# Performance work log

Hardware: AMD Instinct MI355X
Metric: run time of the kernel (lower is better)

The kernel has to match this reference:

```python
import jax, jax.numpy as jnp
import numpy as np

NUM_HEAD = 16
HEAD_DIM = 64
RES_DIM = 1024
LN_EPS = 1e-5


def setup_inputs() -> dict:
    key = jax.random.key(0)
    k1, k2, k3 = jax.random.split(key, 3)
    slen, bsz = 2048, 4
    x = jax.random.normal(k1, (slen, bsz, RES_DIM), dtype=jnp.float32)
    # torch Linear weights: [out_features, in_features]
    w_qkv = jax.random.normal(k2, (NUM_HEAD * 3 * HEAD_DIM, RES_DIM), dtype=jnp.float32) * (1.0 / np.sqrt(RES_DIM))
    w_out = jax.random.normal(k3, (RES_DIM, NUM_HEAD * HEAD_DIM), dtype=jnp.float32) * (1.0 / np.sqrt(NUM_HEAD * HEAD_DIM))
    ln_w = jnp.ones((RES_DIM,), dtype=jnp.float32)
    ln_b = jnp.zeros((RES_DIM,), dtype=jnp.float32)
    return {"x": x, "w_qkv": w_qkv, "w_out": w_out, "ln_w": ln_w, "ln_b": ln_b}


def _layer_norm(x, w, b):
    mu = jnp.mean(x, axis=-1, keepdims=True)
    var = jnp.var(x, axis=-1, keepdims=True)
    return (x - mu) * jax.lax.rsqrt(var + LN_EPS) * w + b


def reference(x, w_qkv, w_out, ln_w, ln_b):
    slen, bsz, _ = x.shape
    scale = 1.0 / np.sqrt(RES_DIM).astype(np.float32)  # note: res_dim, not head_dim
    x_in = _layer_norm(x, ln_w, ln_b)  # pre_lnorm=True
    qkv = x_in @ w_qkv.T  # [s, b, n*3*d]
    qkv = qkv.reshape(slen, bsz, NUM_HEAD, 3 * HEAD_DIM)
    q, k, v = jnp.split(qkv, 3, axis=-1)  # each [s, b, n, d]
    scores = jnp.einsum('ibnd,jbnd->ijbn', q, k) * scale
    attn = jax.nn.softmax(scores, axis=1)  # softmax over keys j
    attn_out = jnp.einsum('ijbn,jbnd->ibnd', attn, v)
    attn_out = attn_out.reshape(slen, bsz, NUM_HEAD * HEAD_DIM)
    attn_out = attn_out @ w_out.T
    return x + attn_out
```

## Files before the change

kernel.cpp:

```cpp
#include <hip/hip_runtime.h>

typedef __bf16 bf16_t;
typedef __bf16 bf16x2 __attribute__((ext_vector_type(2)));
typedef __bf16 bf16x4 __attribute__((ext_vector_type(4)));
typedef __bf16 bf16x8 __attribute__((ext_vector_type(8)));
typedef float f32x4 __attribute__((ext_vector_type(4)));

#define S_LEN 2048
#define BSZ 4
#define NHEAD 16
#define HDIM 64
#define RDIM 1024
#define QKV_N 3072
#define NTOK 8192

__device__ static inline void gload_lds16(const void* g, void* l) {
    __builtin_amdgcn_global_load_lds(
        (const __attribute__((address_space(1))) void*)(unsigned long long)g,
        (__attribute__((address_space(3))) void*)(unsigned long long)l,
        16, 0, 0);
}

__global__ __launch_bounds__(256) void ln_kernel(const float* __restrict__ x,
                                                 const float* __restrict__ lw,
                                                 const float* __restrict__ lb,
                                                 bf16_t* __restrict__ xn) {
    int row = blockIdx.x;
    int tid = threadIdx.x;
    const float4* xr = (const float4*)(x + (size_t)row * RDIM);
    float4 v = xr[tid];
    float s  = v.x + v.y + v.z + v.w;
    float ss = v.x*v.x + v.y*v.y + v.z*v.z + v.w*v.w;
#pragma unroll
    for (int off = 1; off < 64; off <<= 1) {
        s  += __shfl_xor(s, off, 64);
        ss += __shfl_xor(ss, off, 64);
    }
    __shared__ float red[8];
    int wid = tid >> 6, lane = tid & 63;
    if (lane == 0) { red[wid] = s; red[wid + 4] = ss; }
    __syncthreads();
    float S  = red[0] + red[1] + red[2] + red[3];
    float SS = red[4] + red[5] + red[6] + red[7];
    float mu  = S * (1.f / RDIM);
    float var = SS * (1.f / RDIM) - mu * mu;
    float rsig = rsqrtf(var + 1e-5f);
    float4 wv = ((const float4*)lw)[tid];
    float4 bv = ((const float4*)lb)[tid];
    bf16x4 o;
    o[0] = (bf16_t)((v.x - mu) * rsig * wv.x + bv.x);
    o[1] = (bf16_t)((v.y - mu) * rsig * wv.y + bv.y);
    o[2] = (bf16_t)((v.z - mu) * rsig * wv.z + bv.z);
    o[3] = (bf16_t)((v.w - mu) * rsig * wv.w + bv.w);
    *(bf16x4*)(xn + (size_t)row * RDIM + tid * 4) = o;
}

__global__ __launch_bounds__(256) void cvt_kernel(const float* __restrict__ src,
                                                  bf16_t* __restrict__ dst, int n4) {
    int i = blockIdx.x * 256 + threadIdx.x;
    if (i < n4) {
        float4 v = ((const float4*)src)[i];
        bf16x4 o;
        o[0] = (bf16_t)v.x; o[1] = (bf16_t)v.y; o[2] = (bf16_t)v.z; o[3] = (bf16_t)v.w;
        ((bf16x4*)dst)[i] = o;
    }
}

template <int MODE>
__global__ __launch_bounds__(256) void gemm_bt_kernel(const bf16_t* __restrict__ A,
                                                      const bf16_t* __restrict__ Bm,
                                                      bf16_t* __restrict__ Cb,
                                                      const float* __restrict__ X,
                                                      float* __restrict__ Cf,
                                                      int ldc) {
    const int K = 1024;
    __shared__ bf16_t As[128 * 32];
    __shared__ bf16_t Bs[128 * 32];
    int tid = threadIdx.x;
    int lane = tid & 63, wid = tid >> 6;
    int l15 = lane & 15, lg = lane >> 4;
    int wm = wid >> 1, wn = wid & 1;
    int row0 = blockIdx.y * 128;
    int col0 = blockIdx.x * 128;

    int sr = tid >> 2;
    int sc = (tid & 3) * 8;
    const bf16_t* aSrc = A + (size_t)(row0 + sr) * K + sc;
    const bf16_t* bSrc = Bm + (size_t)(col0 + sr) * K + sc;
    bf16_t* aDst = As + tid * 8;
    bf16_t* bDst = Bs + tid * 8;

    f32x4 acc[4][4] = {};
    for (int kt = 0; kt < K; kt += 32) {
        gload_lds16(aSrc + kt, aDst);
        gload_lds16(aSrc + kt + (size_t)64 * K, aDst + 2048);
        gload_lds16(bSrc + kt, bDst);
        gload_lds16(bSrc + kt + (size_t)64 * K, bDst + 2048);
        __syncthreads();
        bf16x8 a[4], b[4];
#pragma unroll
        for (int m = 0; m < 4; m++)
            a[m] = *(const bf16x8*)(As + (wm * 64 + m * 16 + l15) * 32 + lg * 8);
#pragma unroll
        for (int n = 0; n < 4; n++)
            b[n] = *(const bf16x8*)(Bs + (wn * 64 + n * 16 + l15) * 32 + lg * 8);
#pragma unroll
        for (int m = 0; m < 4; m++)
#pragma unroll
            for (int n = 0; n < 4; n++)
                acc[m][n] = __builtin_amdgcn_mfma_f32_16x16x32_bf16(a[m], b[n], acc[m][n], 0, 0, 0);
        __syncthreads();
    }

    int crow = row0 + wm * 64 + lg * 4;
    int ccol = col0 + wn * 64 + l15;
#pragma unroll
    for (int m = 0; m < 4; m++) {
#pragma unroll
        for (int n = 0; n < 4; n++) {
#pragma unroll
            for (int r = 0; r < 4; r++) {
                int rr = crow + m * 16 + r;
                int cc = ccol + n * 16;
                size_t idx = (size_t)rr * ldc + cc;
                if (MODE == 0) {
                    Cb[idx] = (bf16_t)acc[m][n][r];
                } else {
                    Cf[idx] = acc[m][n][r] + X[idx];
                }
            }
        }
    }
}

__global__ __launch_bounds__(256) void attn_kernel(const bf16_t* __restrict__ qkv,
                                                   bf16_t* __restrict__ aout) {
    __shared__ __align__(16) bf16_t Kb[2][4096];
    __shared__ __align__(16) bf16_t VTb[2][64 * 72];
    __shared__ __align__(16) bf16_t Ps[4][16 * 88];
    int tid = threadIdx.x;
    int lane = tid & 63, wid = tid >> 6;
    int l15 = lane & 15, lg = lane >> 4;
    int b = blockIdx.y, h = blockIdx.z;
    int sq = blockIdx.x * 64 + wid * 16 + l15;

    const float scale = 0.03125f;

    const bf16_t* qbase = qkv + (size_t)(sq * 4 + b) * QKV_N + h * 192;
    bf16x8 qf0 = *(const bf16x8*)(qbase + lg * 8);
    bf16x8 qf1 = *(const bf16x8*)(qbase + 32 + lg * 8);

    int kKeyOff = lane >> 3;
    int kChunk  = (lane & 7) ^ (lane >> 3);
    int vr0 = (tid & 31) * 2;
    int vc0 = (tid >> 5) * 8;

    int sw = l15 & 7;
    int koA = ((lg ^ sw)) * 8;
    int koC = (((lg + 4) ^ sw)) * 8;

    float mrun = -3e38f, lrun = 0.f;
    f32x4 o[4] = {};

    {
        const bf16_t* ks = qkv + (size_t)(((0 + wid * 16 + kKeyOff) * 4 + b)) * QKV_N + h * 192 + 64 + kChunk * 8;
        bf16_t* kd = &Kb[0][wid * 1024 + lane * 8];
        gload_lds16(ks, kd);
        gload_lds16(ks + (size_t)8 * 4 * QKV_N, kd + 512);
        const bf16_t* vs = qkv + (size_t)((0 + vr0) * 4 + b) * QKV_N + h * 192 + 128 + vc0;
        bf16x8 v0 = *(const bf16x8*)vs;
        bf16x8 v1 = *(const bf16x8*)(vs + (size_t)4 * QKV_N);
#pragma unroll
        for (int i = 0; i < 8; i++) {
            bf16x2 pr; pr[0] = v0[i]; pr[1] = v1[i];
            *(bf16x2*)(&VTb[0][(vc0 + i) * 72 + vr0]) = pr;
        }
    }
    __syncthreads();

    int cur = 0;
    for (int t = 0; t < S_LEN / 64; t++) {
        bf16x8 v0, v1;
        bool do_stage = (t + 1) < (S_LEN / 64);
        if (do_stage) {
            int kv0 = (t + 1) * 64;
            const bf16_t* ks = qkv + (size_t)(((kv0 + wid * 16 + kKeyOff) * 4 + b)) * QKV_N + h * 192 + 64 + kChunk * 8;
            bf16_t* kd = &Kb[cur ^ 1][wid * 1024 + lane * 8];
            gload_lds16(ks, kd);
            gload_lds16(ks + (size_t)8 * 4 * QKV_N, kd + 512);
            const bf16_t* vs = qkv + (size_t)((kv0 + vr0) * 4 + b) * QKV_N + h * 192 + 128 + vc0;
            v0 = *(const bf16x8*)vs;
            v1 = *(const bf16x8*)(vs + (size_t)4 * QKV_N);
        }

        const bf16_t* kbase = &Kb[cur][l15 * 64];
        bf16x8 kfA[4], kfC[4];
#pragma unroll
        for (int kb = 0; kb < 4; kb++) {
            kfA[kb] = *(const bf16x8*)(kbase + kb * 1024 + koA);
            kfC[kb] = *(const bf16x8*)(kbase + kb * 1024 + koC);
        }
        f32x4 sc4[4];
        __builtin_amdgcn_s_setprio(1);
#pragma unroll
        for (int kb = 0; kb < 4; kb++) {
            f32x4 z = {0.f, 0.f, 0.f, 0.f};
            z = __builtin_amdgcn_mfma_f32_16x16x32_bf16(kfA[kb], qf0, z, 0, 0, 0);
            z = __builtin_amdgcn_mfma_f32_16x16x32_bf16(kfC[kb], qf1, z, 0, 0, 0);
            sc4[kb] = z;
        }
        __builtin_amdgcn_s_setprio(0);

        float tmax = sc4[0][0];
#pragma unroll
        for (int kb = 0; kb < 4; kb++)
#pragma unroll
            for (int r = 0; r < 4; r++) tmax = fmaxf(tmax, sc4[kb][r]);
        tmax = fmaxf(tmax, __shfl_xor(tmax, 16, 64));
        tmax = fmaxf(tmax, __shfl_xor(tmax, 32, 64));
        float mnew = fmaxf(mrun, tmax * scale);
        float corr = __expf(mrun - mnew);
        float lsum = 0.f;
#pragma unroll
        for (int kb = 0; kb < 4; kb++) {
            float p0 = __expf(sc4[kb][0] * scale - mnew);
            float p1 = __expf(sc4[kb][1] * scale - mnew);
            float p2 = __expf(sc4[kb][2] * scale - mnew);
            float p3 = __expf(sc4[kb][3] * scale - mnew);
            lsum += (p0 + p1) + (p2 + p3);
            bf16x4 pw;
            pw[0] = (bf16_t)p0; pw[1] = (bf16_t)p1; pw[2] = (bf16_t)p2; pw[3] = (bf16_t)p3;
            *(bf16x4*)(&Ps[wid][l15 * 88 + kb * 16 + lg * 4]) = pw;
        }
        lsum += __shfl_xor(lsum, 16, 64);
        lsum += __shfl_xor(lsum, 32, 64);
        lrun = lrun * corr + lsum;
        mrun = mnew;
#pragma unroll
        for (int dc = 0; dc < 4; dc++) {
            o[dc][0] *= corr; o[dc][1] *= corr; o[dc][2] *= corr; o[dc][3] *= corr;
        }

        if (do_stage) {
#pragma unroll
            for (int i = 0; i < 8; i++) {
                bf16x2 pr; pr[0] = v0[i]; pr[1] = v1[i];
                *(bf16x2*)(&VTb[cur ^ 1][(vc0 + i) * 72 + vr0]) = pr;
            }
        }

#pragma unroll
        for (int kc = 0; kc < 2; kc++) {
            bf16x8 pf = *(const bf16x8*)(&Ps[wid][l15 * 88 + kc * 32 + lg * 8]);
            __builtin_amdgcn_s_setprio(1);
#pragma unroll
            for (int dc = 0; dc < 4; dc++) {
                bf16x8 vf = *(const bf16x8*)(&VTb[cur][(dc * 16 + l15) * 72 + kc * 32 + lg * 8]);
                o[dc] = __builtin_amdgcn_mfma_f32_16x16x32_bf16(vf, pf, o[dc], 0, 0, 0);
            }
            __builtin_amdgcn_s_setprio(0);
        }

        __syncthreads();
        cur ^= 1;
    }

    float linv = 1.f / lrun;
    bf16_t* ob = aout + (size_t)(sq * 4 + b) * RDIM + h * 64 + lg * 4;
#pragma unroll
    for (int dc = 0; dc < 4; dc++) {
        bf16x4 ov;
        ov[0] = (bf16_t)(o[dc][0] * linv);
        ov[1] = (bf16_t)(o[dc][1] * linv);
        ov[2] = (bf16_t)(o[dc][2] * linv);
        ov[3] = (bf16_t)(o[dc][3] * linv);
        *(bf16x4*)(ob + dc * 16) = ov;
    }
}

extern "C" void kernel_launch(void* const* d_in, const int* in_sizes, int n_in,
                              void* d_out, int out_size, void* d_ws, size_t ws_size,
                              hipStream_t stream) {
    (void)in_sizes; (void)n_in; (void)out_size; (void)ws_size;
    const float* x     = (const float*)d_in[0];
    const float* w_qkv = (const float*)d_in[1];
    const float* w_out = (const float*)d_in[2];
    const float* ln_w  = (const float*)d_in[3];
    const float* ln_b  = (const float*)d_in[4];
    float* out = (float*)d_out;
    char* ws = (char*)d_ws;

    bf16_t* xn      = (bf16_t*)(ws);
    bf16_t* wqkv_bf = (bf16_t*)(ws + 16777216);
    bf16_t* wout_bf = (bf16_t*)(ws + 23068672);
    bf16_t* qkvb    = (bf16_t*)(ws + 25165824);
    bf16_t* attn    = xn;

    ln_kernel<<<NTOK, 256, 0, stream>>>(x, ln_w, ln_b, xn);
    cvt_kernel<<<3072, 256, 0, stream>>>(w_qkv, wqkv_bf, (QKV_N * RDIM) / 4);
    cvt_kernel<<<1024, 256, 0, stream>>>(w_out, wout_bf, (RDIM * RDIM) / 4);

    gemm_bt_kernel<0><<<dim3(QKV_N / 128, NTOK / 128), 256, 0, stream>>>(
        xn, wqkv_bf, qkvb, nullptr, nullptr, QKV_N);

    attn_kernel<<<dim3(S_LEN / 64, BSZ, NHEAD), 256, 0, stream>>>(qkvb, attn);

    gemm_bt_kernel<1><<<dim3(RDIM / 128, NTOK / 128), 256, 0, stream>>>(
        attn, wout_bf, nullptr, x, out, RDIM);
}
```

Measured before the change: 329.0 us.

## Split QKV into head-major K and transposed V layouts written by the GEMM epilogue

The QKV GEMM epilogue now scatters Q to a token-major buffer, K to a per-(batch,head) contiguous layout and V pre-transposed per head. This lets the attention kernel stage both K and V tiles with direct global-to-LDS loads, with no register round-trip or in-kernel transpose. The softmax also switches to exp2 with a folded log2e scale, and the P buffer uses an XOR swizzle instead of padding. The cost is that the V-transposed epilogue writes are strided 2-byte scatters, which may slow the GEMM.

```diff
diff --git a/kernel.cpp b/kernel.cpp
--- a/kernel.cpp
+++ b/kernel.cpp
@@ -69,7 +69,9 @@
 template <int MODE>
 __global__ __launch_bounds__(256) void gemm_bt_kernel(const bf16_t* __restrict__ A,
                                                       const bf16_t* __restrict__ Bm,
-                                                      bf16_t* __restrict__ Cb,
+                                                      bf16_t* __restrict__ Qb,
+                                                      bf16_t* __restrict__ kTd,
+                                                      bf16_t* __restrict__ vTd,
                                                       const float* __restrict__ X,
                                                       float* __restrict__ Cf,
                                                       int ldc) {
@@ -115,82 +117,87 @@
     int crow = row0 + wm * 64 + lg * 4;
     int ccol = col0 + wn * 64 + l15;
 #pragma unroll
-    for (int m = 0; m < 4; m++) {
-#pragma unroll
-        for (int n = 0; n < 4; n++) {
-#pragma unroll
-            for (int r = 0; r < 4; r++) {
-                int rr = crow + m * 16 + r;
-                int cc = ccol + n * 16;
-                size_t idx = (size_t)rr * ldc + cc;
-                if (MODE == 0) {
-                    Cb[idx] = (bf16_t)acc[m][n][r];
-                } else {
-                    Cf[idx] = acc[m][n][r] + X[idx];
+    for (int n = 0; n < 4; n++) {
+        int cc = ccol + n * 16;
+        if (MODE == 0) {
+            int h = cc / 192;
+            int r = cc - h * 192;
+#pragma unroll
+            for (int m = 0; m < 4; m++) {
+#pragma unroll
+                for (int rv = 0; rv < 4; rv++) {
+                    int rr = crow + m * 16 + rv;
+                    bf16_t val = (bf16_t)acc[m][n][rv];
+                    int bb = rr & 3, s = rr >> 2;
+                    if (r < 64) {
+                        Qb[(size_t)rr * RDIM + h * 64 + r] = val;
+                    } else if (r < 128) {
+                        kTd[((size_t)(bb * NHEAD + h) * S_LEN + s) * 64 + (r - 64)] = val;
+                    } else {
+                        vTd[((size_t)(bb * NHEAD + h) * 64 + (r - 128)) * S_LEN + s] = val;
+                    }
                 }
             }
-        }
-    }
-}
-
-__global__ __launch_bounds__(256) void attn_kernel(const bf16_t* __restrict__ qkv,
+        } else {
+#pragma unroll
+            for (int m = 0; m < 4; m++) {
+#pragma unroll
+                for (int rv = 0; rv < 4; rv++) {
+                    int rr = crow + m * 16 + rv;
+                    size_t idx = (size_t)rr * ldc + cc;
+                    Cf[idx] = acc[m][n][rv] + X[idx];
+                }
+            }
+        }
+    }
+}
+
+__global__ __launch_bounds__(256) void attn_kernel(const bf16_t* __restrict__ Qb,
+                                                   const bf16_t* __restrict__ kT,
+                                                   const bf16_t* __restrict__ vT,
                                                    bf16_t* __restrict__ aout) {
     __shared__ __align__(16) bf16_t Kb[2][4096];
-    __shared__ __align__(16) bf16_t VTb[2][64 * 72];
-    __shared__ __align__(16) bf16_t Ps[4][16 * 88];
+    __shared__ __align__(16) bf16_t Vb[2][4096];
+    __shared__ __align__(16) bf16_t Ps[4][1024];
     int tid = threadIdx.x;
     int lane = tid & 63, wid = tid >> 6;
     int l15 = lane & 15, lg = lane >> 4;
     int b = blockIdx.y, h = blockIdx.z;
     int sq = blockIdx.x * 64 + wid * 16 + l15;
 
-    const float scale = 0.03125f;
-
-    const bf16_t* qbase = qkv + (size_t)(sq * 4 + b) * QKV_N + h * 192;
+    const float c2 = 0.04508422002778011f;
+
+    const bf16_t* qbase = Qb + (size_t)(sq * 4 + b) * RDIM + h * 64;
     bf16x8 qf0 = *(const bf16x8*)(qbase + lg * 8);
     bf16x8 qf1 = *(const bf16x8*)(qbase + 32 + lg * 8);
 
-    int kKeyOff = lane >> 3;
-    int kChunk  = (lane & 7) ^ (lane >> 3);
-    int vr0 = (tid & 31) * 2;
-    int vc0 = (tid >> 5) * 8;
+    int srow = tid >> 3, sslot = tid & 7;
+    int sx = sslot ^ (srow & 7);
+    const bf16_t* kS = kT + ((size_t)(b * NHEAD + h) * S_LEN + srow) * 64 + sx * 8;
+    const bf16_t* vS = vT + ((size_t)(b * NHEAD + h) * 64 + srow) * S_LEN + sx * 8;
 
     int sw = l15 & 7;
-    int koA = ((lg ^ sw)) * 8;
-    int koC = (((lg + 4) ^ sw)) * 8;
-
-    float mrun = -3e38f, lrun = 0.f;
+    int koA = (lg ^ sw) * 8;
+    int koC = ((lg + 4) ^ sw) * 8;
+
+    float mh = -3e38f, lrun = 0.f;
     f32x4 o[4] = {};
 
-    {
-        const bf16_t* ks = qkv + (size_t)(((0 + wid * 16 + kKeyOff) * 4 + b)) * QKV_N + h * 192 + 64 + kChunk * 8;
-        bf16_t* kd = &Kb[0][wid * 1024 + lane * 8];
-        gload_lds16(ks, kd);
-        gload_lds16(ks + (size_t)8 * 4 * QKV_N, kd + 512);
-        const bf16_t* vs = qkv + (size_t)((0 + vr0) * 4 + b) * QKV_N + h * 192 + 128 + vc0;
-        bf16x8 v0 = *(const bf16x8*)vs;
-        bf16x8 v1 = *(const bf16x8*)(vs + (size_t)4 * QKV_N);
-#pragma unroll
-        for (int i = 0; i < 8; i++) {
-            bf16x2 pr; pr[0] = v0[i]; pr[1] = v1[i];
-            *(bf16x2*)(&VTb[0][(vc0 + i) * 72 + vr0]) = pr;
-        }
-    }
+    gload_lds16(kS, &Kb[0][tid * 8]);
+    gload_lds16(kS + 32 * 64, &Kb[0][2048 + tid * 8]);
+    gload_lds16(vS, &Vb[0][tid * 8]);
+    gload_lds16(vS + (size_t)32 * S_LEN, &Vb[0][2048 + tid * 8]);
     __syncthreads();
 
     int cur = 0;
     for (int t = 0; t < S_LEN / 64; t++) {
-        bf16x8 v0, v1;
-        bool do_stage = (t + 1) < (S_LEN / 64);
-        if (do_stage) {
-            int kv0 = (t + 1) * 64;
-            const bf16_t* ks = qkv + (size_t)(((kv0 + wid * 16 + kKeyOff) * 4 + b)) * QKV_N + h * 192 + 64 + kChunk * 8;
-            bf16_t* kd = &Kb[cur ^ 1][wid * 1024 + lane * 8];
-            gload_lds16(ks, kd);
-            gload_lds16(ks + (size_t)8 * 4 * QKV_N, kd + 512);
-            const bf16_t* vs = qkv + (size_t)((kv0 + vr0) * 4 + b) * QKV_N + h * 192 + 128 + vc0;
-            v0 = *(const bf16x8*)vs;
-            v1 = *(const bf16x8*)(vs + (size_t)4 * QKV_N);
+        if (t + 1 < S_LEN / 64) {
+            const bf16_t* k2 = kS + (size_t)(t + 1) * 64 * 64;
+            const bf16_t* v2 = vS + (t + 1) * 64;
+            gload_lds16(k2, &Kb[cur ^ 1][tid * 8]);
+            gload_lds16(k2 + 32 * 64, &Kb[cur ^ 1][2048 + tid * 8]);
+            gload_lds16(v2, &Vb[cur ^ 1][tid * 8]);
+            gload_lds16(v2 + (size_t)32 * S_LEN, &Vb[cur ^ 1][2048 + tid * 8]);
         }
 
         const bf16_t* kbase = &Kb[cur][l15 * 64];
@@ -218,44 +225,38 @@
             for (int r = 0; r < 4; r++) tmax = fmaxf(tmax, sc4[kb][r]);
         tmax = fmaxf(tmax, __shfl_xor(tmax, 16, 64));
         tmax = fmaxf(tmax, __shfl_xor(tmax, 32, 64));
-        float mnew = fmaxf(mrun, tmax * scale);
-        float corr = __expf(mrun - mnew);
+        float mn = fmaxf(mh, tmax * c2);
+        float corr = __builtin_amdgcn_exp2f(mh - mn);
         float lsum = 0.f;
 #pragma unroll
         for (int kb = 0; kb < 4; kb++) {
-            float p0 = __expf(sc4[kb][0] * scale - mnew);
-            float p1 = __expf(sc4[kb][1] * scale - mnew);
-            float p2 = __expf(sc4[kb][2] * scale - mnew);
-            float p3 = __expf(sc4[kb][3] * scale - mnew);
+            float p0 = __builtin_amdgcn_exp2f(fmaf(sc4[kb][0], c2, -mn));
+            float p1 = __builtin_amdgcn_exp2f(fmaf(sc4[kb][1], c2, -mn));
+            float p2 = __builtin_amdgcn_exp2f(fmaf(sc4[kb][2], c2, -mn));
+            float p3 = __builtin_amdgcn_exp2f(fmaf(sc4[kb][3], c2, -mn));
             lsum += (p0 + p1) + (p2 + p3);
             bf16x4 pw;
             pw[0] = (bf16_t)p0; pw[1] = (bf16_t)p1; pw[2] = (bf16_t)p2; pw[3] = (bf16_t)p3;
-            *(bf16x4*)(&Ps[wid][l15 * 88 + kb * 16 + lg * 4]) = pw;
+            int j = (kb * 2 + (lg >> 1)) ^ sw;
+            *(bf16x4*)(&Ps[wid][l15 * 64 + j * 8 + (lg & 1) * 4]) = pw;
         }
         lsum += __shfl_xor(lsum, 16, 64);
         lsum += __shfl_xor(lsum, 32, 64);
         lrun = lrun * corr + lsum;
-        mrun = mnew;
+        mh = mn;
 #pragma unroll
         for (int dc = 0; dc < 4; dc++) {
             o[dc][0] *= corr; o[dc][1] *= corr; o[dc][2] *= corr; o[dc][3] *= corr;
         }
 
-        if (do_stage) {
-#pragma unroll
-            for (int i = 0; i < 8; i++) {
-                bf16x2 pr; pr[0] = v0[i]; pr[1] = v1[i];
-                *(bf16x2*)(&VTb[cur ^ 1][(vc0 + i) * 72 + vr0]) = pr;
-            }
-        }
-
 #pragma unroll
         for (int kc = 0; kc < 2; kc++) {
-            bf16x8 pf = *(const bf16x8*)(&Ps[wid][l15 * 88 + kc * 32 + lg * 8]);
+            int cslot = (kc * 4 + lg) ^ sw;
+            bf16x8 pf = *(const bf16x8*)(&Ps[wid][l15 * 64 + cslot * 8]);
             __builtin_amdgcn_s_setprio(1);
 #pragma unroll
             for (int dc = 0; dc < 4; dc++) {
-                bf16x8 vf = *(const bf16x8*)(&VTb[cur][(dc * 16 + l15) * 72 + kc * 32 + lg * 8]);
+                bf16x8 vf = *(const bf16x8*)(&Vb[cur][(dc * 16 + l15) * 64 + cslot * 8]);
                 o[dc] = __builtin_amdgcn_mfma_f32_16x16x32_bf16(vf, pf, o[dc], 0, 0, 0);
             }
             __builtin_amdgcn_s_setprio(0);
@@ -293,7 +294,9 @@
     bf16_t* xn      = (bf16_t*)(ws);
     bf16_t* wqkv_bf = (bf16_t*)(ws + 16777216);
     bf16_t* wout_bf = (bf16_t*)(ws + 23068672);
-    bf16_t* qkvb    = (bf16_t*)(ws + 25165824);
+    bf16_t* Qb      = (bf16_t*)(ws + 25165824);
+    bf16_t* kT      = (bf16_t*)(ws + 41943040);
+    bf16_t* vT      = (bf16_t*)(ws + 58720256);
     bf16_t* attn    = xn;
 
     ln_kernel<<<NTOK, 256, 0, stream>>>(x, ln_w, ln_b, xn);
@@ -301,10 +304,10 @@
     cvt_kernel<<<1024, 256, 0, stream>>>(w_out, wout_bf, (RDIM * RDIM) / 4);
 
     gemm_bt_kernel<0><<<dim3(QKV_N / 128, NTOK / 128), 256, 0, stream>>>(
-        xn, wqkv_bf, qkvb, nullptr, nullptr, QKV_N);
-
-    attn_kernel<<<dim3(S_LEN / 64, BSZ, NHEAD), 256, 0, stream>>>(qkvb, attn);
+        xn, wqkv_bf, Qb, kT, vT, nullptr, nullptr, 0);
+
+    attn_kernel<<<dim3(S_LEN / 64, BSZ, NHEAD), 256, 0, stream>>>(Qb, kT, vT, attn);
 
     gemm_bt_kernel<1><<<dim3(RDIM / 128, NTOK / 128), 256, 0, stream>>>(
-        attn, wout_bf, nullptr, x, out, RDIM);
-}
+        attn, wout_bf, nullptr, nullptr, nullptr, x, out, RDIM);
+}
```

Result: slower. 342.2 us (+4.0%).
